# Kernel optimization log

Hardware: AMD Instinct MI355X
Metric: run time of the kernel (lower is better)

The kernel has to match this reference:

```python
import math
import jax, jax.numpy as jnp
import numpy as np

NEG_INF = -1e9


def maximum_path(neg_cent, text_len, spec_len):
    """Monotonic alignment search (VITS). neg_cent: [B, Ty(spec), Tx(text)].
    Returns hard path [B, Ty, Tx] (float32, 0/1)."""
    B, Ty, Tx = neg_cent.shape
    xs = jnp.arange(Tx)

    # Forward DP over spec frames y; carry = best cumulative value per text pos x.
    def fwd_step(value, inp):
        y, score = inp  # score: [B, Tx]
        diag = jnp.pad(value[:, :-1], ((0, 0), (1, 0)), constant_values=NEG_INF)
        d = diag > value  # move-diagonally indicator for backtracking
        new = score + jnp.maximum(value, diag)
        new = jnp.where(y == 0, jnp.where(xs == 0, score, NEG_INF), new)
        return new, d

    init = jnp.full((B, Tx), NEG_INF, dtype=neg_cent.dtype)
    _, dirs = jax.lax.scan(fwd_step, init,
                           (jnp.arange(Ty), jnp.swapaxes(neg_cent, 0, 1)))
    # dirs: [Ty, B, Tx] bool; dirs[y] compares row y-1 values (as in cython MAS).

    # Backtrack from (spec_len-1, text_len-1) down to y=0.
    def bwd_step(index, inp):
        y, d_row = inp  # index: [B] int32, d_row: [B, Tx]
        active = y < spec_len  # [B]
        row = jnp.where(active[:, None],
                        jax.nn.one_hot(index, Tx, dtype=jnp.float32), 0.0)
        d_at = jnp.take_along_axis(d_row, index[:, None], axis=1)[:, 0]
        move = (index != 0) & ((index == y) | d_at)
        index = jnp.where(active & move, index - 1, index)
        return index, row

    init_idx = text_len - 1
    _, path = jax.lax.scan(bwd_step, init_idx, (jnp.arange(Ty), dirs),
                           reverse=True)
    return jnp.swapaxes(path, 0, 1)  # [B, Ty, Tx]


def setup_inputs() -> dict:
    key = jax.random.key(0)
    ks = jax.random.split(key, 6)
    B, C, Tx, Ty = 8, 192, 512, 2048
    z_p = jax.random.normal(ks[0], (B, C, Ty), dtype=jnp.float32)
    m_p = jax.random.normal(ks[1], (B, C, Tx), dtype=jnp.float32)
    logs_p = 0.1 * jax.random.normal(ks[2], (B, C, Tx), dtype=jnp.float32)
    logs_q = 0.1 * jax.random.normal(ks[3], (B, C, Ty), dtype=jnp.float32)
    text_len = jax.random.randint(ks[4], (B,), Tx * 3 // 4, Tx + 1)
    spec_len = jax.random.randint(ks[5], (B,), Ty * 3 // 4, Ty + 1)
    text_mask = (jnp.arange(Tx)[None, :] < text_len[:, None]).astype(jnp.float32)[:, None, :]
    spec_mask = (jnp.arange(Ty)[None, :] < spec_len[:, None]).astype(jnp.float32)[:, None, :]
    return {"z_p": z_p, "m_p": m_p, "logs_p": logs_p, "logs_q": logs_q,
            "text_mask": text_mask, "spec_mask": spec_mask}


def reference(z_p, m_p, logs_p, logs_q, text_mask, spec_mask):
    text_len = jnp.sum(text_mask, axis=(1, 2)).astype(jnp.int32)  # [B]
    spec_len = jnp.sum(spec_mask, axis=(1, 2)).astype(jnp.int32)  # [B]

    # ---- search_path: neg log-likelihood grid [B, T_spec, T_text] ----
    s_p_sq_r = jnp.exp(-2.0 * logs_p)  # [B, C, Tx]
    nc1 = jnp.sum(-0.5 * math.log(2 * math.pi) - logs_p, axis=1, keepdims=True)  # [B,1,Tx]
    nc2 = jnp.einsum('bct,bcx->btx', -0.5 * z_p * z_p, s_p_sq_r)
    nc3 = jnp.einsum('bct,bcx->btx', z_p, m_p * s_p_sq_r)
    nc4 = jnp.sum(-0.5 * m_p * m_p * s_p_sq_r, axis=1, keepdims=True)  # [B,1,Tx]
    neg_cent = nc1 + nc2 + nc3 + nc4  # [B, Ty, Tx]

    MAS_path = maximum_path(neg_cent, text_len, spec_len)  # [B, Ty, Tx]

    # ---- gather-combine text stats onto spec frames ----
    m_p_a = jnp.einsum('btx,bcx->bct', MAS_path, m_p)      # [B, C, Ty]
    logs_p_a = jnp.einsum('btx,bcx->bct', MAS_path, logs_p)

    # ---- KL divergence loss (VITS) ----
    kl = logs_p_a - logs_q - 0.5 \
        + 0.5 * jnp.square(z_p - m_p_a) * jnp.exp(-2.0 * logs_p_a)
    loss_kl = jnp.sum(kl * spec_mask) / jnp.sum(spec_mask)

    duration = jnp.sum(MAS_path, axis=1)[:, None, :]  # [B, 1, Tx]
    return MAS_path[:, None], m_p_a, logs_p_a, loss_kl, duration
```

## Files before the change

### kernel.cpp

```cpp
#include <hip/hip_runtime.h>
#include <cstdint>
#include <cstddef>

#define BB 8
#define CC 192
#define TXX 512
#define TYY 2048

#define NEG_INF (-1e9f)
#define HALF_LOG_2PI 0.9189385332046727f

#define O1 8388608
#define O2 11534336
#define O3 14680064
#define O4 14680065

#define WS_NEG   0
#define WS_S     33554432
#define WS_MSR   36700160
#define WS_BIAS  39845888
#define WS_DIRS  39862272
#define WS_IDX   40910848
#define WS_LENS  40976384
#define WS_PART  40976448

typedef float f32x4 __attribute__((ext_vector_type(4)));

__global__ void k_zero(float* __restrict__ out) {
    int64_t i = (int64_t)blockIdx.x * blockDim.x + threadIdx.x;
    const int64_t n4 = (int64_t)BB * TYY * TXX / 4;
    float4 z4 = make_float4(0.f, 0.f, 0.f, 0.f);
    float4* p4 = (float4*)out;
    for (int64_t k = i; k < n4; k += (int64_t)gridDim.x * blockDim.x) p4[k] = z4;
    if (i < BB * TXX) out[O4 + i] = 0.0f;
}

__global__ void k_prep(const float* __restrict__ logs_p, const float* __restrict__ m_p,
                       float* __restrict__ s, float* __restrict__ msr) {
    int i = blockIdx.x * blockDim.x + threadIdx.x;
    float lp = logs_p[i], m = m_p[i];
    float sv = expf(-2.0f * lp);
    s[i] = sv;
    msr[i] = m * sv;
}

__global__ void k_bias(const float* __restrict__ logs_p, const float* __restrict__ m_p,
                       const float* __restrict__ msr, float* __restrict__ bias) {
    int i = blockIdx.x * blockDim.x + threadIdx.x;
    int b = i >> 9, x = i & (TXX - 1);
    size_t base = (size_t)b * CC * TXX + x;
    const float* lpb = logs_p + base;
    const float* mb  = m_p + base;
    const float* msb = msr + base;
    float acc = 0.f;
#pragma unroll 8
    for (int c = 0; c < CC; ++c)
        acc += -HALF_LOG_2PI - lpb[(size_t)c * TXX] - 0.5f * mb[(size_t)c * TXX] * msb[(size_t)c * TXX];
    bias[i] = acc;
}

__global__ void k_len(const float* __restrict__ tmask, const float* __restrict__ smask,
                      int* __restrict__ lens) {
    __shared__ float red[256];
    int b = blockIdx.x, tid = threadIdx.x;
    float ts = 0.f;
    for (int i = tid; i < TXX; i += 256) ts += tmask[b * TXX + i];
    red[tid] = ts; __syncthreads();
    for (int s = 128; s > 0; s >>= 1) { if (tid < s) red[tid] += red[tid + s]; __syncthreads(); }
    if (tid == 0) lens[b] = (int)(red[0] + 0.5f);
    __syncthreads();
    float ss = 0.f;
    for (int i = tid; i < TYY; i += 256) ss += smask[b * TYY + i];
    red[tid] = ss; __syncthreads();
    for (int s = 128; s > 0; s >>= 1) { if (tid < s) red[tid] += red[tid + s]; __syncthreads(); }
    if (tid == 0) lens[8 + b] = (int)(red[0] + 0.5f);
}

__global__ __launch_bounds__(256) void k_gemm(const float* __restrict__ z,
                                              const float* __restrict__ msr,
                                              const float* __restrict__ sarr,
                                              const float* __restrict__ bias,
                                              const int* __restrict__ lens,
                                              float* __restrict__ neg) {
    int x0 = blockIdx.x * 64, t0 = blockIdx.y * 64, b = blockIdx.z;
    if (x0 >= lens[b] || t0 >= lens[8 + b]) return;

    __shared__ float Zs[16][68], Ms[16][68], Ss[16][68];
    int tid = threadIdx.x;
    int tx = tid & 15, ty = tid >> 4;
    const float* zb = z    + (size_t)b * CC * TYY;
    const float* mb = msr  + (size_t)b * CC * TXX;
    const float* sb = sarr + (size_t)b * CC * TXX;
    int lr = tid >> 4, lc = (tid & 15) * 4;
    float acc[4][4] = {};
    for (int k0 = 0; k0 < CC; k0 += 16) {
        float4 zv = *(const float4*)(zb + (size_t)(k0 + lr) * TYY + t0 + lc);
        float4 mv = *(const float4*)(mb + (size_t)(k0 + lr) * TXX + x0 + lc);
        float4 sv = *(const float4*)(sb + (size_t)(k0 + lr) * TXX + x0 + lc);
        __syncthreads();
        *(float4*)&Zs[lr][lc] = zv;
        *(float4*)&Ms[lr][lc] = mv;
        *(float4*)&Ss[lr][lc] = sv;
        __syncthreads();
#pragma unroll
        for (int k = 0; k < 16; ++k) {
            float4 a4  = *(const float4*)&Zs[k][ty * 4];
            float4 bm4 = *(const float4*)&Ms[k][tx * 4];
            float4 bs4 = *(const float4*)&Ss[k][tx * 4];
            float av[4]  = {a4.x, a4.y, a4.z, a4.w};
            float bmv[4] = {bm4.x, bm4.y, bm4.z, bm4.w};
            float bsv[4] = {bs4.x, bs4.y, bs4.z, bs4.w};
#pragma unroll
            for (int i2 = 0; i2 < 4; ++i2) {
                float a2 = -0.5f * av[i2] * av[i2];
#pragma unroll
                for (int j = 0; j < 4; ++j)
                    acc[i2][j] += av[i2] * bmv[j] + a2 * bsv[j];
            }
        }
    }
    float4 b4 = *(const float4*)(bias + b * TXX + x0 + tx * 4);
    float bv[4] = {b4.x, b4.y, b4.z, b4.w};
#pragma unroll
    for (int i2 = 0; i2 < 4; ++i2) {
        int t = t0 + ty * 4 + i2;
        float4 o;
        o.x = acc[i2][0] + bv[0]; o.y = acc[i2][1] + bv[1];
        o.z = acc[i2][2] + bv[2]; o.w = acc[i2][3] + bv[3];
        *(float4*)(neg + ((size_t)b * TYY + t) * TXX + x0 + tx * 4) = o;
    }
}

#define GLOAD4(DST, PTR, OFF)                                             \
    asm volatile("global_load_dwordx4 %0, %1, off offset:" #OFF           \
                 : "=v"(DST) : "v"(PTR) : "memory")

#define WAIT_VM(N) do {                                                   \
    asm volatile("s_waitcnt vmcnt(" #N ")" ::: "memory");                 \
    __builtin_amdgcn_sched_barrier(0);                                    \
} while (0)

#define LOADG(DST, G) do {                                                \
    const char* p0_ = (const char*)nc4 + (size_t)(G) * 16384 + lane * 32; \
    const char* p2_ = p0_ + 4096;                                         \
    const char* p4_ = p0_ + 8192;                                         \
    const char* p6_ = p0_ + 12288;                                        \
    GLOAD4(DST[0],  p0_, 0);    GLOAD4(DST[1],  p0_, 16);                 \
    GLOAD4(DST[2],  p0_, 2048); GLOAD4(DST[3],  p0_, 2064);               \
    GLOAD4(DST[4],  p2_, 0);    GLOAD4(DST[5],  p2_, 16);                 \
    GLOAD4(DST[6],  p2_, 2048); GLOAD4(DST[7],  p2_, 2064);               \
    GLOAD4(DST[8],  p4_, 0);    GLOAD4(DST[9],  p4_, 16);                 \
    GLOAD4(DST[10], p4_, 2048); GLOAD4(DST[11], p4_, 2064);               \
    GLOAD4(DST[12], p6_, 0);    GLOAD4(DST[13], p6_, 16);                 \
    GLOAD4(DST[14], p6_, 2048); GLOAD4(DST[15], p6_, 2064);               \
} while (0)

#define DPROW(CUR, YB, R) do {                                                \
    int y_ = (YB) + (R);                                                      \
    float s0_ = CUR[2*(R)][0],   s1_ = CUR[2*(R)][1];                         \
    float s2_ = CUR[2*(R)][2],   s3_ = CUR[2*(R)][3];                         \
    float s4_ = CUR[2*(R)+1][0], s5_ = CUR[2*(R)+1][1];                       \
    float s6_ = CUR[2*(R)+1][2], s7_ = CUR[2*(R)+1][3];                       \
    unsigned d_ = 0;                                                          \
    if (y_ == 0) {                                                            \
        if (lane == 0) v[0] = s0_;             \
    } else {                                                                  \
        float pl_ = __int_as_float(__builtin_amdgcn_update_dpp(               \
            0, __float_as_int(v[7]), 0x138, 0xF, 0xF, false));                \
        if (lane == 0) pl_ = NEG_INF;                                         \
        float n0_ = s0_ + fmaxf(v[0], pl_);  if (pl_  > v[0]) d_ |= 1u;       \
        float n1_ = s1_ + fmaxf(v[1], v[0]); if (v[0] > v[1]) d_ |= 2u;       \
        float n2_ = s2_ + fmaxf(v[2], v[1]); if (v[1] > v[2]) d_ |= 4u;       \
        float n3_ = s3_ + fmaxf(v[3], v[2]); if (v[2] > v[3]) d_ |= 8u;       \
        float n4_ = s4_ + fmaxf(v[4], v[3]); if (v[3] > v[4]) d_ |= 16u;      \
        float n5_ = s5_ + fmaxf(v[5], v[4]); if (v[4] > v[5]) d_ |= 32u;      \
        float n6_ = s6_ + fmaxf(v[6], v[5]); if (v[5] > v[6]) d_ |= 64u;      \
        float n7_ = s7_ + fmaxf(v[7], v[6]); if (v[6] > v[7]) d_ |= 128u;     \
        v[0] = n0_; v[1] = n1_; v[2] = n2_; v[3] = n3_;                       \
        v[4] = n4_; v[5] = n5_; v[6] = n6_; v[7] = n7_;                       \
    }                                                                         \
    unsigned t_ = (unsigned)(y_ - 8 * lane);                                  \
    if (t_ < 8u) d_ |= 1u << t_;                 \
    acc |= d_ << (((R) & 3) * 8);                                             \
    if (((R) & 3) == 3) { db32[(y_ >> 2) * 64 + lane] = acc; acc = 0; }       \
} while (0)

#define FWD_ITER(G, CUR, NXT) do {                                \
    int g_ = (G);                                                 \
    if (g_ + 2 < ng) {                                            \
        LOADG(NXT, g_ + 2);                 \
        WAIT_VM(32);                                              \
    } else if (g_ + 1 < ng) {                                     \
        WAIT_VM(16);                                              \
    } else {                                                      \
        WAIT_VM(0);                                               \
    }                                                             \
    int yb_ = 8 * g_;                                             \
    DPROW(CUR, yb_, 0); DPROW(CUR, yb_, 1);                       \
    DPROW(CUR, yb_, 2); DPROW(CUR, yb_, 3);                       \
    DPROW(CUR, yb_, 4); DPROW(CUR, yb_, 5);                       \
    DPROW(CUR, yb_, 6); DPROW(CUR, yb_, 7);                       \
} while (0)

__global__ __launch_bounds__(64, 1) void k_fwd(const float* __restrict__ neg,
                                               const int* __restrict__ lens,
                                               uint32_t* __restrict__ dirs) {
    int b = blockIdx.x, lane = threadIdx.x;
    const float* nc4 = neg + (size_t)b * TYY * TXX;
    uint32_t* db32 = dirs + (size_t)b * (TYY / 4) * 64;
    int slen = lens[8 + b];
    int ng = (slen + 7) >> 3;

    float v[8];
#pragma unroll
    for (int j = 0; j < 8; ++j) v[j] = NEG_INF;
    unsigned acc = 0;

    f32x4 bufA[16], bufB[16], bufC[16];
    LOADG(bufA, 0);
    LOADG(bufB, 1);

    for (int p = 0; p < ng; p += 3) {
        FWD_ITER(p, bufA, bufC);
        if (p + 1 < ng) FWD_ITER(p + 1, bufB, bufA);
        if (p + 2 < ng) FWD_ITER(p + 2, bufC, bufB);
    }
}

__global__ __launch_bounds__(64, 1) void k_bwd(const int* __restrict__ lens,
                                               const uint32_t* __restrict__ dirs,
                                               int* __restrict__ idx_map) {
    int b = blockIdx.x, lane = threadIdx.x;
    const uint32_t* db32 = dirs + (size_t)b * (TYY / 4) * 64;
    int tlen = lens[b], slen = lens[8 + b];

    int idx = tlen - 1;
    int y0 = slen - 1;
    while (y0 >= 0) {
        int nsteps = (y0 + 1 < 32) ? y0 + 1 : 32;
        int y = y0 - lane;
        int yy = (y < 0) ? 0 : y;
        int w0 = (idx >> 5) - 1;
        if (w0 < 0) w0 = 0;
        if (w0 > 14) w0 = 14;
        int qrow = (yy >> 2) * 64;
        int byteoff = (yy & 3) * 8;
        uint32_t lo = 0, hi = 0;
        if (lane < 32) {
#pragma unroll
            for (int k = 0; k < 4; ++k)
                lo |= ((db32[qrow + 4 * w0 + k] >> byteoff) & 0xffu) << (8 * k);
#pragma unroll
            for (int k = 0; k < 4; ++k)
                hi |= ((db32[qrow + 4 * w0 + 4 + k] >> byteoff) & 0xffu) << (8 * k);
        }
        int base = w0 << 5;
        int cap = 0;
#pragma unroll
        for (int j = 0; j < 32; ++j) {
            if (lane == j) cap = idx;
            uint32_t l = (uint32_t)__builtin_amdgcn_readlane((int)lo, j);
            uint32_t h = (uint32_t)__builtin_amdgcn_readlane((int)hi, j);
            int bp = idx - base;
            uint32_t word = (bp & 32) ? h : l;
            int bit = (int)((word >> (bp & 31)) & 1u);
            int move = (int)(idx != 0) & bit;
            idx -= move;
        }
        if (lane < nsteps) idx_map[b * TYY + (y0 - lane)] = cap;
        y0 -= 32;
    }
}

__global__ void k_scatter(const int* __restrict__ lens, const int* __restrict__ idx_map,
                          float* __restrict__ out) {
    int i = blockIdx.x * blockDim.x + threadIdx.x;
    int b = i >> 11, y = i & (TYY - 1);
    if (y < lens[8 + b]) {
        int x = idx_map[i];
        out[(size_t)i * TXX + x] = 1.0f;
        atomicAdd(&out[O4 + b * TXX + x], 1.0f);
    }
}

__global__ __launch_bounds__(256) void k_gather(const float* __restrict__ z_p,
                                                const float* __restrict__ m_p,
                                                const float* __restrict__ logs_p,
                                                const float* __restrict__ logs_q,
                                                const int* __restrict__ lens,
                                                const int* __restrict__ idx_map,
                                                float* __restrict__ out,
                                                float* __restrict__ partials) {
    const int S = BB * CC * TYY / 4;
    int base = blockIdx.x * 256 + threadIdx.x;
    float klsum = 0.f;
#pragma unroll
    for (int r = 0; r < 4; ++r) {
        int i = base + r * S;
        int t = i & (TYY - 1);
        int bc = i >> 11;
        int b = bc / CC;
        float ma = 0.f, la = 0.f;
        if (t < lens[8 + b]) {
            int x = idx_map[b * TYY + t];
            size_t off = (size_t)bc * TXX + x;
            ma = m_p[off];
            la = logs_p[off];
            float zv = z_p[i], lq = logs_q[i];
            float dz = zv - ma;
            klsum += la - lq - 0.5f + 0.5f * dz * dz * expf(-2.0f * la);
        }
        out[O1 + i] = ma;
        out[O2 + i] = la;
    }
    for (int o = 32; o > 0; o >>= 1) klsum += __shfl_down(klsum, o);
    __shared__ float red[4];
    if ((threadIdx.x & 63) == 0) red[threadIdx.x >> 6] = klsum;
    __syncthreads();
    if (threadIdx.x == 0) partials[blockIdx.x] = red[0] + red[1] + red[2] + red[3];
}

__global__ void k_final(const float* __restrict__ partials, const int* __restrict__ lens,
                        float* __restrict__ out) {
    float s = 0.f;
    for (int i = threadIdx.x; i < 3072; i += 256) s += partials[i];
    for (int o = 32; o > 0; o >>= 1) s += __shfl_down(s, o);
    __shared__ float red[4];
    if ((threadIdx.x & 63) == 0) red[threadIdx.x >> 6] = s;
    __syncthreads();
    if (threadIdx.x == 0) {
        float tot = 0.f;
        for (int b = 0; b < 8; ++b) tot += (float)lens[8 + b];
        out[O3] = (red[0] + red[1] + red[2] + red[3]) / tot;
    }
}

extern "C" void kernel_launch(void* const* d_in, const int* in_sizes, int n_in,
                              void* d_out, int out_size, void* d_ws, size_t ws_size,
                              hipStream_t stream) {
    const float* z_p    = (const float*)d_in[0];
    const float* m_p    = (const float*)d_in[1];
    const float* logs_p = (const float*)d_in[2];
    const float* logs_q = (const float*)d_in[3];
    const float* tmask  = (const float*)d_in[4];
    const float* smask  = (const float*)d_in[5];
    float* out = (float*)d_out;
    char* ws = (char*)d_ws;

    float*    neg      = (float*)(ws + WS_NEG);
    float*    sarr     = (float*)(ws + WS_S);
    float*    msr      = (float*)(ws + WS_MSR);
    float*    bias     = (float*)(ws + WS_BIAS);
    uint32_t* dirs     = (uint32_t*)(ws + WS_DIRS);
    int*      idx_map  = (int*)(ws + WS_IDX);
    int*      lens     = (int*)(ws + WS_LENS);
    float*    partials = (float*)(ws + WS_PART);

    hipLaunchKernelGGL(k_zero,    dim3(2048),      dim3(256), 0, stream, out);
    hipLaunchKernelGGL(k_prep,    dim3(3072),      dim3(256), 0, stream, logs_p, m_p, sarr, msr);
    hipLaunchKernelGGL(k_bias,    dim3(64),        dim3(64),  0, stream, logs_p, m_p, msr, bias);
    hipLaunchKernelGGL(k_len,     dim3(8),         dim3(256), 0, stream, tmask, smask, lens);
    hipLaunchKernelGGL(k_gemm,    dim3(8, 32, 8),  dim3(256), 0, stream, z_p, msr, sarr, bias, lens, neg);
    hipLaunchKernelGGL(k_fwd,     dim3(8),         dim3(64),  0, stream, neg, lens, dirs);
    hipLaunchKernelGGL(k_bwd,     dim3(8),         dim3(64),  0, stream, lens, dirs, idx_map);
    hipLaunchKernelGGL(k_scatter, dim3(64),        dim3(256), 0, stream, lens, idx_map, out);
    hipLaunchKernelGGL(k_gather,  dim3(3072),      dim3(256), 0, stream, z_p, m_p, logs_p, logs_q,
                       lens, idx_map, out, partials);
    hipLaunchKernelGGL(k_final,   dim3(1),         dim3(256), 0, stream, partials, lens, out);
}
```

Baseline: 563.1 us.

## Fuse preprocessing kernels, prefetch backtrack direction words, fold scatter into backtrack

Merges the zero, prep, bias and length kernels into one block-partitioned launch, with bias recomputing exp locally so it no longer depends on msr. Fuses the path scatter and duration atomics into the backtrack kernel, which drops a launch. Restructures backtrack to prefetch the next 32-row window of direction bytes (three words) while the current chunk is processed, hiding load latency on the serial critical path. It also drops the idx!=0 guard, on the assumption that direction bits at x=0 are never set.

```diff
diff --git a/kernel.cpp b/kernel.cpp
--- a/kernel.cpp
+++ b/kernel.cpp
@@ -26,54 +26,63 @@
 
 typedef float f32x4 __attribute__((ext_vector_type(4)));
 
-__global__ void k_zero(float* __restrict__ out) {
-    int64_t i = (int64_t)blockIdx.x * blockDim.x + threadIdx.x;
-    const int64_t n4 = (int64_t)BB * TYY * TXX / 4;
-    float4 z4 = make_float4(0.f, 0.f, 0.f, 0.f);
-    float4* p4 = (float4*)out;
-    for (int64_t k = i; k < n4; k += (int64_t)gridDim.x * blockDim.x) p4[k] = z4;
-    if (i < BB * TXX) out[O4 + i] = 0.0f;
-}
-
-__global__ void k_prep(const float* __restrict__ logs_p, const float* __restrict__ m_p,
-                       float* __restrict__ s, float* __restrict__ msr) {
-    int i = blockIdx.x * blockDim.x + threadIdx.x;
-    float lp = logs_p[i], m = m_p[i];
-    float sv = expf(-2.0f * lp);
-    s[i] = sv;
-    msr[i] = m * sv;
-}
-
-__global__ void k_bias(const float* __restrict__ logs_p, const float* __restrict__ m_p,
-                       const float* __restrict__ msr, float* __restrict__ bias) {
-    int i = blockIdx.x * blockDim.x + threadIdx.x;
-    int b = i >> 9, x = i & (TXX - 1);
-    size_t base = (size_t)b * CC * TXX + x;
-    const float* lpb = logs_p + base;
-    const float* mb  = m_p + base;
-    const float* msb = msr + base;
-    float acc = 0.f;
+#define PRE_NZERO 2048
+#define PRE_NPREP 3072
+#define PRE_NBIAS 16
+#define PRE_NLEN  8
+__global__ __launch_bounds__(256) void k_pre(const float* __restrict__ logs_p,
+                                             const float* __restrict__ m_p,
+                                             const float* __restrict__ tmask,
+                                             const float* __restrict__ smask,
+                                             float* __restrict__ s,
+                                             float* __restrict__ msr,
+                                             float* __restrict__ bias,
+                                             int* __restrict__ lens,
+                                             float* __restrict__ out) {
+    int blk = blockIdx.x, tid = threadIdx.x;
+    if (blk < PRE_NZERO) {
+        int64_t i = (int64_t)blk * 256 + tid;
+        const int64_t n4 = (int64_t)BB * TYY * TXX / 4;
+        float4 z4 = make_float4(0.f, 0.f, 0.f, 0.f);
+        float4* p4 = (float4*)out;
+        for (int64_t k = i; k < n4; k += (int64_t)PRE_NZERO * 256) p4[k] = z4;
+        if (i < BB * TXX) out[O4 + i] = 0.0f;
+    } else if (blk < PRE_NZERO + PRE_NPREP) {
+        int i = (blk - PRE_NZERO) * 256 + tid;
+        float lp = logs_p[i], m = m_p[i];
+        float sv = expf(-2.0f * lp);
+        s[i] = sv;
+        msr[i] = m * sv;
+    } else if (blk < PRE_NZERO + PRE_NPREP + PRE_NBIAS) {
+        int i = (blk - PRE_NZERO - PRE_NPREP) * 256 + tid;
+        int b = i >> 9, x = i & (TXX - 1);
+        size_t base = (size_t)b * CC * TXX + x;
+        const float* lpb = logs_p + base;
+        const float* mb  = m_p + base;
+        float acc = 0.f;
 #pragma unroll 8
-    for (int c = 0; c < CC; ++c)
-        acc += -HALF_LOG_2PI - lpb[(size_t)c * TXX] - 0.5f * mb[(size_t)c * TXX] * msb[(size_t)c * TXX];
-    bias[i] = acc;
-}
-
-__global__ void k_len(const float* __restrict__ tmask, const float* __restrict__ smask,
-                      int* __restrict__ lens) {
-    __shared__ float red[256];
-    int b = blockIdx.x, tid = threadIdx.x;
-    float ts = 0.f;
-    for (int i = tid; i < TXX; i += 256) ts += tmask[b * TXX + i];
-    red[tid] = ts; __syncthreads();
-    for (int s = 128; s > 0; s >>= 1) { if (tid < s) red[tid] += red[tid + s]; __syncthreads(); }
-    if (tid == 0) lens[b] = (int)(red[0] + 0.5f);
-    __syncthreads();
-    float ss = 0.f;
-    for (int i = tid; i < TYY; i += 256) ss += smask[b * TYY + i];
-    red[tid] = ss; __syncthreads();
-    for (int s = 128; s > 0; s >>= 1) { if (tid < s) red[tid] += red[tid + s]; __syncthreads(); }
-    if (tid == 0) lens[8 + b] = (int)(red[0] + 0.5f);
+        for (int c = 0; c < CC; ++c) {
+            float lp = lpb[(size_t)c * TXX];
+            float m  = mb[(size_t)c * TXX];
+            float msv = m * expf(-2.0f * lp);
+            acc += -HALF_LOG_2PI - lp - 0.5f * m * msv;
+        }
+        bias[i] = acc;
+    } else {
+        __shared__ float red[256];
+        int b = blk - (PRE_NZERO + PRE_NPREP + PRE_NBIAS);
+        float ts = 0.f;
+        for (int i = tid; i < TXX; i += 256) ts += tmask[b * TXX + i];
+        red[tid] = ts; __syncthreads();
+        for (int s2 = 128; s2 > 0; s2 >>= 1) { if (tid < s2) red[tid] += red[tid + s2]; __syncthreads(); }
+        if (tid == 0) lens[b] = (int)(red[0] + 0.5f);
+        __syncthreads();
+        float ss = 0.f;
+        for (int i = tid; i < TYY; i += 256) ss += smask[b * TYY + i];
+        red[tid] = ss; __syncthreads();
+        for (int s2 = 128; s2 > 0; s2 >>= 1) { if (tid < s2) red[tid] += red[tid + s2]; __syncthreads(); }
+        if (tid == 0) lens[8 + b] = (int)(red[0] + 0.5f);
+    }
 }
 
 __global__ __launch_bounds__(256) void k_gemm(const float* __restrict__ z,
@@ -227,34 +236,53 @@
     }
 }
 
+#define LOADW(D0, D1, D2, WB, QROW, BOFF) do {                            \
+    const uint32_t* p_ = db32 + (QROW) + 4 * (WB);                        \
+    uint32_t a0_=p_[0], a1_=p_[1], a2_=p_[2],  a3_=p_[3];                 \
+    uint32_t b0_=p_[4], b1_=p_[5], b2_=p_[6],  b3_=p_[7];                 \
+    uint32_t c0_=p_[8], c1_=p_[9], c2_=p_[10], c3_=p_[11];                \
+    D0 = ((a0_>>(BOFF))&0xffu)        | (((a1_>>(BOFF))&0xffu)<<8) |      \
+         (((a2_>>(BOFF))&0xffu)<<16)  | (((a3_>>(BOFF))&0xffu)<<24);      \
+    D1 = ((b0_>>(BOFF))&0xffu)        | (((b1_>>(BOFF))&0xffu)<<8) |      \
+         (((b2_>>(BOFF))&0xffu)<<16)  | (((b3_>>(BOFF))&0xffu)<<24);      \
+    D2 = ((c0_>>(BOFF))&0xffu)        | (((c1_>>(BOFF))&0xffu)<<8) |      \
+         (((c2_>>(BOFF))&0xffu)<<16)  | (((c3_>>(BOFF))&0xffu)<<24);      \
+} while (0)
+
 __global__ __launch_bounds__(64, 1) void k_bwd(const int* __restrict__ lens,
                                                const uint32_t* __restrict__ dirs,
-                                               int* __restrict__ idx_map) {
+                                               int* __restrict__ idx_map,
+                                               float* __restrict__ out) {
     int b = blockIdx.x, lane = threadIdx.x;
     const uint32_t* db32 = dirs + (size_t)b * (TYY / 4) * 64;
     int tlen = lens[b], slen = lens[8 + b];
 
     int idx = tlen - 1;
     int y0 = slen - 1;
+    int wb;
+    uint32_t W0 = 0, W1 = 0, W2 = 0;
+    {
+        int yy = y0 - lane; if (yy < 0) yy = 0;
+        int qrow = (yy >> 2) * 64, boff = (yy & 3) * 8;
+        int t = (idx >> 5) - 1; if (t < 0) t = 0; if (t > 13) t = 13;
+        wb = t;
+        if (lane < 32) LOADW(W0, W1, W2, wb, qrow, boff);
+    }
     while (y0 >= 0) {
+        int w0 = (idx >> 5) - 1; if (w0 < 0) w0 = 0; if (w0 > 14) w0 = 14;
+        int s = w0 - wb; if (s < 0) s = 0; if (s > 1) s = 1;
+        uint32_t lo = s ? W1 : W0;
+        uint32_t hi = s ? W2 : W1;
+        int base = (wb + s) << 5;
+        uint32_t N0 = 0, N1 = 0, N2 = 0;
+        int idxm = idx - 32; if (idxm < 0) idxm = 0;
+        int wbn = (idxm >> 5) - 1; if (wbn < 0) wbn = 0; if (wbn > 13) wbn = 13;
+        {
+            int yn = y0 - 32 - lane; if (yn < 0) yn = 0;
+            int qn = (yn >> 2) * 64, bn = (yn & 3) * 8;
+            if (lane < 32) LOADW(N0, N1, N2, wbn, qn, bn);
+        }
         int nsteps = (y0 + 1 < 32) ? y0 + 1 : 32;
-        int y = y0 - lane;
-        int yy = (y < 0) ? 0 : y;
-        int w0 = (idx >> 5) - 1;
-        if (w0 < 0) w0 = 0;
-        if (w0 > 14) w0 = 14;
-        int qrow = (yy >> 2) * 64;
-        int byteoff = (yy & 3) * 8;
-        uint32_t lo = 0, hi = 0;
-        if (lane < 32) {
-#pragma unroll
-            for (int k = 0; k < 4; ++k)
-                lo |= ((db32[qrow + 4 * w0 + k] >> byteoff) & 0xffu) << (8 * k);
-#pragma unroll
-            for (int k = 0; k < 4; ++k)
-                hi |= ((db32[qrow + 4 * w0 + 4 + k] >> byteoff) & 0xffu) << (8 * k);
-        }
-        int base = w0 << 5;
         int cap = 0;
 #pragma unroll
         for (int j = 0; j < 32; ++j) {
@@ -263,23 +291,16 @@
             uint32_t h = (uint32_t)__builtin_amdgcn_readlane((int)hi, j);
             int bp = idx - base;
             uint32_t word = (bp & 32) ? h : l;
-            int bit = (int)((word >> (bp & 31)) & 1u);
-            int move = (int)(idx != 0) & bit;
-            idx -= move;
-        }
-        if (lane < nsteps) idx_map[b * TYY + (y0 - lane)] = cap;
+            idx -= (int)((word >> (bp & 31)) & 1u);
+        }
+        if (lane < nsteps) {
+            int y = y0 - lane;
+            idx_map[b * TYY + y] = cap;
+            out[((size_t)(b * TYY + y)) * TXX + cap] = 1.0f;
+            atomicAdd(&out[O4 + b * TXX + cap], 1.0f);
+        }
+        wb = wbn; W0 = N0; W1 = N1; W2 = N2;
         y0 -= 32;
-    }
-}
-
-__global__ void k_scatter(const int* __restrict__ lens, const int* __restrict__ idx_map,
-                          float* __restrict__ out) {
-    int i = blockIdx.x * blockDim.x + threadIdx.x;
-    int b = i >> 11, y = i & (TYY - 1);
-    if (y < lens[8 + b]) {
-        int x = idx_map[i];
-        out[(size_t)i * TXX + x] = 1.0f;
-        atomicAdd(&out[O4 + b * TXX + x], 1.0f);
     }
 }
 
@@ -356,15 +377,14 @@
     int*      lens     = (int*)(ws + WS_LENS);
     float*    partials = (float*)(ws + WS_PART);
 
-    hipLaunchKernelGGL(k_zero,    dim3(2048),      dim3(256), 0, stream, out);
-    hipLaunchKernelGGL(k_prep,    dim3(3072),      dim3(256), 0, stream, logs_p, m_p, sarr, msr);
-    hipLaunchKernelGGL(k_bias,    dim3(64),        dim3(64),  0, stream, logs_p, m_p, msr, bias);
-    hipLaunchKernelGGL(k_len,     dim3(8),         dim3(256), 0, stream, tmask, smask, lens);
-    hipLaunchKernelGGL(k_gemm,    dim3(8, 32, 8),  dim3(256), 0, stream, z_p, msr, sarr, bias, lens, neg);
-    hipLaunchKernelGGL(k_fwd,     dim3(8),         dim3(64),  0, stream, neg, lens, dirs);
-    hipLaunchKernelGGL(k_bwd,     dim3(8),         dim3(64),  0, stream, lens, dirs, idx_map);
-    hipLaunchKernelGGL(k_scatter, dim3(64),        dim3(256), 0, stream, lens, idx_map, out);
-    hipLaunchKernelGGL(k_gather,  dim3(3072),      dim3(256), 0, stream, z_p, m_p, logs_p, logs_q,
-                       lens, idx_map, out, partials);
-    hipLaunchKernelGGL(k_final,   dim3(1),         dim3(256), 0, stream, partials, lens, out);
-}
+    hipLaunchKernelGGL(k_pre, dim3(PRE_NZERO + PRE_NPREP + PRE_NBIAS + PRE_NLEN),
+                       dim3(256), 0, stream,
+                       logs_p, m_p, tmask, smask, sarr, msr, bias, lens, out);
+    hipLaunchKernelGGL(k_gemm,   dim3(8, 32, 8), dim3(256), 0, stream,
+                       z_p, msr, sarr, bias, lens, neg);
+    hipLaunchKernelGGL(k_fwd,    dim3(8),        dim3(64),  0, stream, neg, lens, dirs);
+    hipLaunchKernelGGL(k_bwd,    dim3(8),        dim3(64),  0, stream, lens, dirs, idx_map, out);
+    hipLaunchKernelGGL(k_gather, dim3(3072),     dim3(256), 0, stream,
+                       z_p, m_p, logs_p, logs_q, lens, idx_map, out, partials);
+    hipLaunchKernelGGL(k_final,  dim3(1),        dim3(256), 0, stream, partials, lens, out);
+}
```

Result: faster. 525.4 us (-6.7%).
